# Kernel tuning notes

Measured on AMD Instinct MI355X. Metric: run time of the kernel, lower is better.

## Reference

```python
import jax, jax.numpy as jnp
import numpy as np

N = 100000   # nodes
E = 1600000  # edges
F_IN = 32    # num_features
H = 16       # hidden_size (hardcoded as conv2 input in source)
C = 10       # num_classes
K = 2        # kernel_size (dim=1)


def setup_inputs() -> dict:
    key = jax.random.key(0)
    ks = jax.random.split(key, 9)
    x = jax.random.normal(ks[0], (N, F_IN), dtype=jnp.float32)
    edge_index = jax.random.randint(ks[1], (2, E), 0, N, dtype=jnp.int64)
    edge_attr = jax.random.uniform(ks[2], (E, 1), dtype=jnp.float32)
    s1 = 1.0 / np.sqrt(F_IN)
    s2 = 1.0 / np.sqrt(H)
    W1 = jax.random.normal(ks[3], (K, F_IN, H), dtype=jnp.float32) * s1
    root1 = jax.random.normal(ks[4], (F_IN, H), dtype=jnp.float32) * s1
    b1 = jnp.zeros((H,), dtype=jnp.float32)
    W2 = jax.random.normal(ks[5], (K, H, C), dtype=jnp.float32) * s2
    root2 = jax.random.normal(ks[6], (H, C), dtype=jnp.float32) * s2
    b2 = jnp.zeros((C,), dtype=jnp.float32)
    return {"x": x, "edge_index": edge_index, "edge_attr": edge_attr,
            "W1": W1, "root1": root1, "b1": b1,
            "W2": W2, "root2": root2, "b2": b2}


def spline_conv(x, edge_index, edge_attr, W, root, bias, num_nodes):
    # Open B-spline, degree 1: hat-function basis over K knots.
    k = W.shape[0]
    src, dst = edge_index[0], edge_index[1]
    v = edge_attr[:, 0] * (k - 1)                                   # [E]
    grid = jnp.arange(k, dtype=v.dtype)
    basis = jnp.maximum(0.0, 1.0 - jnp.abs(v[:, None] - grid[None, :]))  # [E,K]
    xe = x[src]                                                      # [E,in] gather
    msg = jnp.einsum('ei,kio,ek->eo', xe, W, basis)                  # per-edge message
    agg = jax.ops.segment_sum(msg, dst, num_segments=num_nodes)      # scatter-add
    deg = jax.ops.segment_sum(jnp.ones((msg.shape[0],), x.dtype), dst,
                              num_segments=num_nodes)
    agg = agg / jnp.maximum(deg, 1.0)[:, None]                       # mean aggregation
    return agg + x @ root + bias


def reference(x, edge_index, edge_attr, W1, root1, b1, W2, root2, b2):
    # Inference mode: F.dropout(training=False) is identity.
    h = jax.nn.elu(spline_conv(x, edge_index, edge_attr, W1, root1, b1, N))
    out = spline_conv(h, edge_index, edge_attr, W2, root2, b2, N)
    return jax.nn.log_softmax(out, axis=1)
```

## Files before the change

### kernel.cpp

```cpp
#include <hip/hip_runtime.h>
#include <math.h>

#define N_NODES 100000
#define E_EDGES 1600000
#define F_IN 32
#define HID 16
#define NC 10
#define SRC_BITS 17
#define SRC_MASK ((1u << SRC_BITS) - 1u)
#define VQ_SCALE 32767.0f
#define CBITS 9
#define BUCKET_N 512
#define NCB ((N_NODES + BUCKET_N - 1) / BUCKET_N)
#define BLK_E 4096
#define NBLK ((E_EDGES + BLK_E - 1) / BLK_E)
#define NODE_GRID ((N_NODES + 255) / 256)

__device__ __forceinline__ unsigned int bf16pair(float lo, float hi) {
    unsigned int ulo = __float_as_uint(lo), uhi = __float_as_uint(hi);
    ulo += 0x7fffu + ((ulo >> 16) & 1u);
    uhi += 0x7fffu + ((uhi >> 16) & 1u);
    return (ulo >> 16) | (uhi & 0xffff0000u);
}

__device__ __forceinline__ float lerp_pair(unsigned int pair, float v) {
    float a = __uint_as_float(pair << 16);
    float b = __uint_as_float(pair & 0xffff0000u);
    return fmaf(v, b - a, a);
}

__global__ __launch_bounds__(256) void fused_l1cnt(
    const float* __restrict__ x, const float* __restrict__ W1,
    const float* __restrict__ root1, const float* __restrict__ b1,
    const int* __restrict__ ei,
    unsigned int* __restrict__ y, float* __restrict__ r1,
    int* __restrict__ cnt)
{
    if (blockIdx.x >= NODE_GRID) {
        __shared__ int h[NCB];
        int b = blockIdx.x - NODE_GRID;
        for (int i = threadIdx.x; i < NCB; i += 256) h[i] = 0;
        __syncthreads();
        int e0 = b * BLK_E;
        for (int i = threadIdx.x; i < BLK_E; i += 256) {
            int e = e0 + i;
            if (e < E_EDGES) atomicAdd(&h[ei[E_EDGES + e] >> CBITS], 1);
        }
        __syncthreads();
        for (int s = threadIdx.x; s < NCB; s += 256)
            cnt[s * NBLK + b] = h[s];
        return;
    }
    __shared__ float sW0[F_IN * HID], sW1[F_IN * HID], sR[F_IN * HID], sB[HID];
    for (int i = threadIdx.x; i < F_IN * HID; i += 256) {
        sW0[i] = W1[i];
        sW1[i] = W1[F_IN * HID + i];
        sR[i]  = root1[i];
    }
    if (threadIdx.x < HID) sB[threadIdx.x] = b1[threadIdx.x];
    __syncthreads();

    int n = blockIdx.x * 256 + threadIdx.x;
    if (n >= N_NODES) return;

    float xr[F_IN];
    const float4* xp = (const float4*)(x + (size_t)n * F_IN);
    #pragma unroll
    for (int i = 0; i < F_IN / 4; i++) {
        float4 t = xp[i];
        xr[i*4+0] = t.x; xr[i*4+1] = t.y; xr[i*4+2] = t.z; xr[i*4+3] = t.w;
    }

    float a0[HID], a1[HID], ar[HID];
    #pragma unroll
    for (int o = 0; o < HID; o++) { a0[o] = 0.f; a1[o] = 0.f; ar[o] = sB[o]; }
    for (int i = 0; i < F_IN; i++) {
        float xi = xr[i];
        #pragma unroll
        for (int o = 0; o < HID; o++) {
            a0[o] += xi * sW0[i * HID + o];
            a1[o] += xi * sW1[i * HID + o];
            ar[o] += xi * sR[i * HID + o];
        }
    }
    unsigned int* py = y + (size_t)n * 16;
    float* pr = r1 + (size_t)n * HID;
    #pragma unroll
    for (int o = 0; o < HID; o++) {
        py[o] = bf16pair(a0[o], a1[o]);
        pr[o] = ar[o];
    }
}

__global__ __launch_bounds__(512) void k_cscan(int* __restrict__ cnt,
                                               int* __restrict__ tsum,
                                               int* __restrict__ start)
{
    __shared__ int lds[512];
    int s = blockIdx.x, t = threadIdx.x;
    int v = (t < NBLK) ? cnt[s * NBLK + t] : 0;
    lds[t] = v;
    __syncthreads();
    #pragma unroll
    for (int off = 1; off < 512; off <<= 1) {
        int u = (t >= off) ? lds[t - off] : 0;
        __syncthreads();
        lds[t] += u;
        __syncthreads();
    }
    if (t < NBLK) cnt[s * NBLK + t] = lds[t] - v;
    if (t == 511) tsum[s] = lds[511];
    if (s == 0 && t == 0) start[N_NODES] = E_EDGES;
}

__global__ __launch_bounds__(256) void k_bucket(
    const int* __restrict__ ei, const float* __restrict__ ea,
    const int* __restrict__ pref, const int* __restrict__ tsum,
    int2* __restrict__ ebuf)
{
    __shared__ int sbb[256];
    __shared__ int base[NCB], cur[NCB];
    int t = threadIdx.x;
    int v = (t < NCB) ? tsum[t] : 0;
    sbb[t] = v;
    __syncthreads();
    #pragma unroll
    for (int off = 1; off < 256; off <<= 1) {
        int u = (t >= off) ? sbb[t - off] : 0;
        __syncthreads();
        sbb[t] += u;
        __syncthreads();
    }
    if (t < NCB) {
        base[t] = (sbb[t] - v) + pref[t * NBLK + blockIdx.x];
        cur[t] = 0;
    }
    __syncthreads();
    int e0 = blockIdx.x * BLK_E;
    for (int i = t; i < BLK_E; i += 256) {
        int e = e0 + i;
        if (e >= E_EDGES) continue;
        int dst = ei[E_EDGES + e];
        int s = dst >> CBITS;
        int off = atomicAdd(&cur[s], 1);
        unsigned int vq = (unsigned int)(ea[e] * VQ_SCALE + 0.5f);
        unsigned int packed = (vq << SRC_BITS) | (unsigned int)ei[e];
        ebuf[base[s] + off] = make_int2(dst & (BUCKET_N - 1), (int)packed);
    }
}

__global__ __launch_bounds__(512) void k_bsort(
    const int2* __restrict__ ebuf, const int* __restrict__ tsum,
    unsigned int* __restrict__ es, int* __restrict__ start)
{
    __shared__ int sbb[256];
    __shared__ int hist[BUCKET_N];
    __shared__ int cursor[BUCKET_N];
    __shared__ int wsum[8], woff[8];
    int t = threadIdx.x;
    int b = blockIdx.x;
    int v = 0;
    if (t < 256) { v = (t < NCB) ? tsum[t] : 0; sbb[t] = v; }
    __syncthreads();
    #pragma unroll
    for (int off = 1; off < 256; off <<= 1) {
        int u = 0;
        if (t < 256 && t >= off) u = sbb[t - off];
        __syncthreads();
        if (t < 256) sbb[t] += u;
        __syncthreads();
    }
    int m  = tsum[b];
    int j0 = sbb[b] - m;
    int j1 = j0 + m;
    hist[t] = 0; cursor[t] = 0;
    __syncthreads();
    for (int j = j0 + t; j < j1; j += 512)
        atomicAdd(&hist[ebuf[j].x], 1);
    __syncthreads();
    int c = hist[t];
    int w = t >> 6, l = t & 63;
    int incl = c;
    #pragma unroll
    for (int off = 1; off < 64; off <<= 1) {
        int u = __shfl_up(incl, off, 64);
        if (l >= off) incl += u;
    }
    if (l == 63) wsum[w] = incl;
    __syncthreads();
    if (t == 0) {
        int acc = 0;
        #pragma unroll
        for (int i = 0; i < 8; i++) { woff[i] = acc; acc += wsum[i]; }
    }
    __syncthreads();
    int excl = woff[w] + incl - c;
    hist[t] = excl;
    int node = (b << CBITS) + t;
    if (node < N_NODES) start[node] = j0 + excl;
    __syncthreads();
    for (int j = j0 + t; j < j1; j += 512) {
        int2 p = ebuf[j];
        int off = atomicAdd(&cursor[p.x], 1);
        es[j0 + hist[p.x] + off] = (unsigned int)p.y;
    }
}

__global__ __launch_bounds__(256) void k_agg1(
    const unsigned int* __restrict__ es, const int* __restrict__ start,
    const unsigned int* __restrict__ y, const float* __restrict__ r1,
    const float* __restrict__ W2, const float* __restrict__ root2,
    const float* __restrict__ b2,
    unsigned int* __restrict__ z, float* __restrict__ r2)
{
    __shared__ float sh[16 * 17];
    __shared__ float sW0[HID * NC], sW1[HID * NC], sRt[HID * NC], sB2[NC];
    int t = threadIdx.x;
    if (t < HID * NC) { sW0[t] = W2[t]; sW1[t] = W2[HID * NC + t]; sRt[t] = root2[t]; }
    if (t >= HID * NC && t < HID * NC + NC) sB2[t - HID * NC] = b2[t - HID * NC];

    int idx = blockIdx.x * 256 + t;
    int n = idx >> 4, o = idx & 15, g = t >> 4;
    if (n < N_NODES) {
        int j0 = start[n], j1 = start[n + 1];
        float acc0 = 0.f, acc1 = 0.f, acc2 = 0.f, acc3 = 0.f;
        int j = j0;
        for (; j + 7 < j1; j += 8) {
            unsigned int p0 = es[j],   p1 = es[j+1], p2 = es[j+2], p3 = es[j+3];
            unsigned int p4 = es[j+4], p5 = es[j+5], p6 = es[j+6], p7 = es[j+7];
            unsigned int q0 = y[(size_t)(p0 & SRC_MASK) * 16 + o];
            unsigned int q1 = y[(size_t)(p1 & SRC_MASK) * 16 + o];
            unsigned int q2 = y[(size_t)(p2 & SRC_MASK) * 16 + o];
            unsigned int q3 = y[(size_t)(p3 & SRC_MASK) * 16 + o];
            unsigned int q4 = y[(size_t)(p4 & SRC_MASK) * 16 + o];
            unsigned int q5 = y[(size_t)(p5 & SRC_MASK) * 16 + o];
            unsigned int q6 = y[(size_t)(p6 & SRC_MASK) * 16 + o];
            unsigned int q7 = y[(size_t)(p7 & SRC_MASK) * 16 + o];
            acc0 += lerp_pair(q0, (float)(p0 >> SRC_BITS) * (1.0f / VQ_SCALE));
            acc1 += lerp_pair(q1, (float)(p1 >> SRC_BITS) * (1.0f / VQ_SCALE));
            acc2 += lerp_pair(q2, (float)(p2 >> SRC_BITS) * (1.0f / VQ_SCALE));
            acc3 += lerp_pair(q3, (float)(p3 >> SRC_BITS) * (1.0f / VQ_SCALE));
            acc0 += lerp_pair(q4, (float)(p4 >> SRC_BITS) * (1.0f / VQ_SCALE));
            acc1 += lerp_pair(q5, (float)(p5 >> SRC_BITS) * (1.0f / VQ_SCALE));
            acc2 += lerp_pair(q6, (float)(p6 >> SRC_BITS) * (1.0f / VQ_SCALE));
            acc3 += lerp_pair(q7, (float)(p7 >> SRC_BITS) * (1.0f / VQ_SCALE));
        }
        for (; j + 3 < j1; j += 4) {
            unsigned int p0 = es[j], p1 = es[j+1], p2 = es[j+2], p3 = es[j+3];
            unsigned int q0 = y[(size_t)(p0 & SRC_MASK) * 16 + o];
            unsigned int q1 = y[(size_t)(p1 & SRC_MASK) * 16 + o];
            unsigned int q2 = y[(size_t)(p2 & SRC_MASK) * 16 + o];
            unsigned int q3 = y[(size_t)(p3 & SRC_MASK) * 16 + o];
            acc0 += lerp_pair(q0, (float)(p0 >> SRC_BITS) * (1.0f / VQ_SCALE));
            acc1 += lerp_pair(q1, (float)(p1 >> SRC_BITS) * (1.0f / VQ_SCALE));
            acc2 += lerp_pair(q2, (float)(p2 >> SRC_BITS) * (1.0f / VQ_SCALE));
            acc3 += lerp_pair(q3, (float)(p3 >> SRC_BITS) * (1.0f / VQ_SCALE));
        }
        for (; j < j1; j++) {
            unsigned int p = es[j];
            unsigned int q = y[(size_t)(p & SRC_MASK) * 16 + o];
            acc0 += lerp_pair(q, (float)(p >> SRC_BITS) * (1.0f / VQ_SCALE));
        }
        float acc = (acc0 + acc1) + (acc2 + acc3);
        float inv = 1.0f / fmaxf((float)(j1 - j0), 1.0f);
        float hv = acc * inv + r1[(size_t)n * HID + o];
        sh[g * 17 + o] = hv > 0.0f ? hv : expm1f(hv);
    }
    __syncthreads();

    int n2 = blockIdx.x * 16 + g;
    if (n2 < N_NODES) {
        int cc = o;
        unsigned int* pz = z + (size_t)n2 * 16;
        if (cc < NC) {
            float a0 = 0.f, a1 = 0.f, ar = sB2[cc];
            #pragma unroll
            for (int i = 0; i < HID; i++) {
                float hi = sh[g * 17 + i];
                a0 += hi * sW0[i * NC + cc];
                a1 += hi * sW1[i * NC + cc];
                ar += hi * sRt[i * NC + cc];
            }
            pz[cc] = bf16pair(a0, a1);
            r2[(size_t)n2 * NC + cc] = ar;
        } else {
            pz[cc] = 0u;
        }
    }
}

__global__ __launch_bounds__(256) void k_agg2(
    const unsigned int* __restrict__ es, const int* __restrict__ start,
    const unsigned int* __restrict__ z,
    const float* __restrict__ r2, float* __restrict__ out)
{
    int idx = blockIdx.x * 256 + threadIdx.x;
    int n = idx >> 4, o = idx & 15;
    if (n >= N_NODES) return;
    int j0 = start[n], j1 = start[n + 1];
    float acc0 = 0.f, acc1 = 0.f, acc2 = 0.f, acc3 = 0.f;
    int j = j0;
    for (; j + 7 < j1; j += 8) {
        unsigned int p0 = es[j],   p1 = es[j+1], p2 = es[j+2], p3 = es[j+3];
        unsigned int p4 = es[j+4], p5 = es[j+5], p6 = es[j+6], p7 = es[j+7];
        unsigned int q0 = z[(size_t)(p0 & SRC_MASK) * 16 + o];
        unsigned int q1 = z[(size_t)(p1 & SRC_MASK) * 16 + o];
        unsigned int q2 = z[(size_t)(p2 & SRC_MASK) * 16 + o];
        unsigned int q3 = z[(size_t)(p3 & SRC_MASK) * 16 + o];
        unsigned int q4 = z[(size_t)(p4 & SRC_MASK) * 16 + o];
        unsigned int q5 = z[(size_t)(p5 & SRC_MASK) * 16 + o];
        unsigned int q6 = z[(size_t)(p6 & SRC_MASK) * 16 + o];
        unsigned int q7 = z[(size_t)(p7 & SRC_MASK) * 16 + o];
        acc0 += lerp_pair(q0, (float)(p0 >> SRC_BITS) * (1.0f / VQ_SCALE));
        acc1 += lerp_pair(q1, (float)(p1 >> SRC_BITS) * (1.0f / VQ_SCALE));
        acc2 += lerp_pair(q2, (float)(p2 >> SRC_BITS) * (1.0f / VQ_SCALE));
        acc3 += lerp_pair(q3, (float)(p3 >> SRC_BITS) * (1.0f / VQ_SCALE));
        acc0 += lerp_pair(q4, (float)(p4 >> SRC_BITS) * (1.0f / VQ_SCALE));
        acc1 += lerp_pair(q5, (float)(p5 >> SRC_BITS) * (1.0f / VQ_SCALE));
        acc2 += lerp_pair(q6, (float)(p6 >> SRC_BITS) * (1.0f / VQ_SCALE));
        acc3 += lerp_pair(q7, (float)(p7 >> SRC_BITS) * (1.0f / VQ_SCALE));
    }
    for (; j + 3 < j1; j += 4) {
        unsigned int p0 = es[j], p1 = es[j+1], p2 = es[j+2], p3 = es[j+3];
        unsigned int q0 = z[(size_t)(p0 & SRC_MASK) * 16 + o];
        unsigned int q1 = z[(size_t)(p1 & SRC_MASK) * 16 + o];
        unsigned int q2 = z[(size_t)(p2 & SRC_MASK) * 16 + o];
        unsigned int q3 = z[(size_t)(p3 & SRC_MASK) * 16 + o];
        acc0 += lerp_pair(q0, (float)(p0 >> SRC_BITS) * (1.0f / VQ_SCALE));
        acc1 += lerp_pair(q1, (float)(p1 >> SRC_BITS) * (1.0f / VQ_SCALE));
        acc2 += lerp_pair(q2, (float)(p2 >> SRC_BITS) * (1.0f / VQ_SCALE));
        acc3 += lerp_pair(q3, (float)(p3 >> SRC_BITS) * (1.0f / VQ_SCALE));
    }
    for (; j < j1; j++) {
        unsigned int p = es[j];
        unsigned int q = z[(size_t)(p & SRC_MASK) * 16 + o];
        acc0 += lerp_pair(q, (float)(p >> SRC_BITS) * (1.0f / VQ_SCALE));
    }
    float acc = (acc0 + acc1) + (acc2 + acc3);
    float val = -INFINITY;
    if (o < NC) {
        float inv = 1.0f / fmaxf((float)(j1 - j0), 1.0f);
        val = acc * inv + r2[(size_t)n * NC + o];
    }
    float mx = val;
    #pragma unroll
    for (int off = 8; off > 0; off >>= 1) mx = fmaxf(mx, __shfl_xor(mx, off, 16));
    float ex = (o < NC) ? expf(val - mx) : 0.0f;
    float ssum = ex;
    #pragma unroll
    for (int off = 8; off > 0; off >>= 1) ssum += __shfl_xor(ssum, off, 16);
    if (o < NC) out[(size_t)n * NC + o] = val - mx - logf(ssum);
}

extern "C" void kernel_launch(void* const* d_in, const int* in_sizes, int n_in,
                              void* d_out, int out_size, void* d_ws, size_t ws_size,
                              hipStream_t stream) {
    const float* x     = (const float*)d_in[0];
    const int*   ei    = (const int*)d_in[1];
    const float* ea    = (const float*)d_in[2];
    const float* W1    = (const float*)d_in[3];
    const float* root1 = (const float*)d_in[4];
    const float* b1    = (const float*)d_in[5];
    const float* W2    = (const float*)d_in[6];
    const float* root2 = (const float*)d_in[7];
    const float* b2    = (const float*)d_in[8];
    float* out = (float*)d_out;

    char* wsb = (char*)d_ws;
    int2*         ebuf   = (int2*)wsb;
    unsigned int* es     = (unsigned int*)(wsb + (size_t)E_EDGES * 8);
    unsigned int* y      = es + (size_t)E_EDGES;
    float*        r1     = (float*)(y + (size_t)N_NODES * 16);
    unsigned int* z      = (unsigned int*)(r1 + (size_t)N_NODES * HID);
    float*        r2     = (float*)(z + (size_t)N_NODES * 16);
    int*          start  = (int*)(r2 + (size_t)N_NODES * NC);
    int*          cnt    = start + N_NODES + 1;
    int*          tsum   = cnt + NCB * NBLK;

    int aggGrid  = (N_NODES * 16 + 255) / 256;

    fused_l1cnt<<<NODE_GRID + NBLK, 256, 0, stream>>>(x, W1, root1, b1, ei, y, r1, cnt);
    k_cscan <<<NCB, 512, 0, stream>>>(cnt, tsum, start);
    k_bucket<<<NBLK, 256, 0, stream>>>(ei, ea, cnt, tsum, ebuf);
    k_bsort <<<NCB, 512, 0, stream>>>(ebuf, tsum, es, start);
    k_agg1  <<<aggGrid, 256, 0, stream>>>(es, start, y, r1, W2, root2, b2, z, r2);
    k_agg2  <<<aggGrid, 256, 0, stream>>>(es, start, z, r2, out);
}
```

Before: 191.8 us.

## Vectorize edge loads, double bucket block size, use wave-shuffle scans

Doubles the per-block edge chunk of the bucket/count passes so there are half as many blocks and prefix entries (NBLK drops to fit 256 threads). The count and bucket kernels read dst, src and edge_attr with 128-bit int4/float4 loads, four edges per thread. The LDS Hillis-Steele scans in k_cscan, k_bucket and k_bsort become wave-level __shfl_up scans plus a small cross-wave combine, cutting barrier count. The bigger blocks mean fewer blocks for the bucket pass, which may lower occupancy and raise LDS atomic contention per block.

```diff
diff --git a/kernel.cpp b/kernel.cpp
--- a/kernel.cpp
+++ b/kernel.cpp
@@ -12,7 +12,7 @@
 #define CBITS 9
 #define BUCKET_N 512
 #define NCB ((N_NODES + BUCKET_N - 1) / BUCKET_N)
-#define BLK_E 4096
+#define BLK_E 8192
 #define NBLK ((E_EDGES + BLK_E - 1) / BLK_E)
 #define NODE_GRID ((N_NODES + 255) / 256)
 
@@ -41,10 +41,20 @@
         int b = blockIdx.x - NODE_GRID;
         for (int i = threadIdx.x; i < NCB; i += 256) h[i] = 0;
         __syncthreads();
+        const int* dstp = ei + E_EDGES;
         int e0 = b * BLK_E;
-        for (int i = threadIdx.x; i < BLK_E; i += 256) {
+        for (int i = threadIdx.x * 4; i < BLK_E; i += 1024) {
             int e = e0 + i;
-            if (e < E_EDGES) atomicAdd(&h[ei[E_EDGES + e] >> CBITS], 1);
+            if (e + 3 < E_EDGES) {
+                int4 d4 = *(const int4*)(dstp + e);
+                atomicAdd(&h[d4.x >> CBITS], 1);
+                atomicAdd(&h[d4.y >> CBITS], 1);
+                atomicAdd(&h[d4.z >> CBITS], 1);
+                atomicAdd(&h[d4.w >> CBITS], 1);
+            } else {
+                for (int k = 0; k < 4; k++)
+                    if (e + k < E_EDGES) atomicAdd(&h[dstp[e + k] >> CBITS], 1);
+            }
         }
         __syncthreads();
         for (int s = threadIdx.x; s < NCB; s += 256)
@@ -92,24 +102,31 @@
     }
 }
 
-__global__ __launch_bounds__(512) void k_cscan(int* __restrict__ cnt,
+__global__ __launch_bounds__(256) void k_cscan(int* __restrict__ cnt,
                                                int* __restrict__ tsum,
                                                int* __restrict__ start)
 {
-    __shared__ int lds[512];
+    __shared__ int wsum[4], woff[4];
     int s = blockIdx.x, t = threadIdx.x;
     int v = (t < NBLK) ? cnt[s * NBLK + t] : 0;
-    lds[t] = v;
-    __syncthreads();
-    #pragma unroll
-    for (int off = 1; off < 512; off <<= 1) {
-        int u = (t >= off) ? lds[t - off] : 0;
-        __syncthreads();
-        lds[t] += u;
-        __syncthreads();
-    }
-    if (t < NBLK) cnt[s * NBLK + t] = lds[t] - v;
-    if (t == 511) tsum[s] = lds[511];
+    int w = t >> 6, l = t & 63;
+    int incl = v;
+    #pragma unroll
+    for (int off = 1; off < 64; off <<= 1) {
+        int u = __shfl_up(incl, off, 64);
+        if (l >= off) incl += u;
+    }
+    if (l == 63) wsum[w] = incl;
+    __syncthreads();
+    if (t == 0) {
+        int a = 0;
+        #pragma unroll
+        for (int i = 0; i < 4; i++) { woff[i] = a; a += wsum[i]; }
+    }
+    __syncthreads();
+    int excl = woff[w] + incl - v;
+    if (t < NBLK) cnt[s * NBLK + t] = excl;
+    if (t == 255) tsum[s] = woff[3] + incl;
     if (s == 0 && t == 0) start[N_NODES] = E_EDGES;
 }
 
@@ -118,34 +135,79 @@
     const int* __restrict__ pref, const int* __restrict__ tsum,
     int2* __restrict__ ebuf)
 {
-    __shared__ int sbb[256];
+    __shared__ int wsum[4], woff[4];
     __shared__ int base[NCB], cur[NCB];
     int t = threadIdx.x;
     int v = (t < NCB) ? tsum[t] : 0;
-    sbb[t] = v;
-    __syncthreads();
-    #pragma unroll
-    for (int off = 1; off < 256; off <<= 1) {
-        int u = (t >= off) ? sbb[t - off] : 0;
-        __syncthreads();
-        sbb[t] += u;
-        __syncthreads();
-    }
+    int w = t >> 6, l = t & 63;
+    int incl = v;
+    #pragma unroll
+    for (int off = 1; off < 64; off <<= 1) {
+        int u = __shfl_up(incl, off, 64);
+        if (l >= off) incl += u;
+    }
+    if (l == 63) wsum[w] = incl;
+    __syncthreads();
+    if (t == 0) {
+        int a = 0;
+        #pragma unroll
+        for (int i = 0; i < 4; i++) { woff[i] = a; a += wsum[i]; }
+    }
+    __syncthreads();
     if (t < NCB) {
-        base[t] = (sbb[t] - v) + pref[t * NBLK + blockIdx.x];
+        base[t] = (woff[w] + incl - v) + pref[t * NBLK + blockIdx.x];
         cur[t] = 0;
     }
     __syncthreads();
+
+    const int* dstp = ei + E_EDGES;
     int e0 = blockIdx.x * BLK_E;
-    for (int i = t; i < BLK_E; i += 256) {
+    for (int i = t * 4; i < BLK_E; i += 1024) {
         int e = e0 + i;
-        if (e >= E_EDGES) continue;
-        int dst = ei[E_EDGES + e];
-        int s = dst >> CBITS;
-        int off = atomicAdd(&cur[s], 1);
-        unsigned int vq = (unsigned int)(ea[e] * VQ_SCALE + 0.5f);
-        unsigned int packed = (vq << SRC_BITS) | (unsigned int)ei[e];
-        ebuf[base[s] + off] = make_int2(dst & (BUCKET_N - 1), (int)packed);
+        if (e + 3 < E_EDGES) {
+            int4 d4 = *(const int4*)(dstp + e);
+            int4 s4 = *(const int4*)(ei + e);
+            float4 a4 = *(const float4*)(ea + e);
+            {
+                int s = d4.x >> CBITS;
+                int off = atomicAdd(&cur[s], 1);
+                unsigned int vq = (unsigned int)(a4.x * VQ_SCALE + 0.5f);
+                ebuf[base[s] + off] = make_int2(d4.x & (BUCKET_N - 1),
+                                               (int)((vq << SRC_BITS) | (unsigned int)s4.x));
+            }
+            {
+                int s = d4.y >> CBITS;
+                int off = atomicAdd(&cur[s], 1);
+                unsigned int vq = (unsigned int)(a4.y * VQ_SCALE + 0.5f);
+                ebuf[base[s] + off] = make_int2(d4.y & (BUCKET_N - 1),
+                                               (int)((vq << SRC_BITS) | (unsigned int)s4.y));
+            }
+            {
+                int s = d4.z >> CBITS;
+                int off = atomicAdd(&cur[s], 1);
+                unsigned int vq = (unsigned int)(a4.z * VQ_SCALE + 0.5f);
+                ebuf[base[s] + off] = make_int2(d4.z & (BUCKET_N - 1),
+                                               (int)((vq << SRC_BITS) | (unsigned int)s4.z));
+            }
+            {
+                int s = d4.w >> CBITS;
+                int off = atomicAdd(&cur[s], 1);
+                unsigned int vq = (unsigned int)(a4.w * VQ_SCALE + 0.5f);
+                ebuf[base[s] + off] = make_int2(d4.w & (BUCKET_N - 1),
+                                               (int)((vq << SRC_BITS) | (unsigned int)s4.w));
+            }
+        } else {
+            for (int k = 0; k < 4; k++) {
+                int ee = e + k;
+                if (ee >= E_EDGES) break;
+                int dst = dstp[ee];
+                int s = dst >> CBITS;
+                int off = atomicAdd(&cur[s], 1);
+                unsigned int vq = (unsigned int)(ea[ee] * VQ_SCALE + 0.5f);
+                ebuf[base[s] + off] = make_int2(dst & (BUCKET_N - 1),
+                                               (int)((vq << SRC_BITS) | (unsigned int)ei[ee]));
+            }
+        }
     }
 }
 
@@ -153,28 +215,35 @@
     const int2* __restrict__ ebuf, const int* __restrict__ tsum,
     unsigned int* __restrict__ es, int* __restrict__ start)
 {
-    __shared__ int sbb[256];
     __shared__ int hist[BUCKET_N];
     __shared__ int cursor[BUCKET_N];
     __shared__ int wsum[8], woff[8];
+    __shared__ int sj0;
     int t = threadIdx.x;
     int b = blockIdx.x;
-    int v = 0;
-    if (t < 256) { v = (t < NCB) ? tsum[t] : 0; sbb[t] = v; }
-    __syncthreads();
-    #pragma unroll
-    for (int off = 1; off < 256; off <<= 1) {
-        int u = 0;
-        if (t < 256 && t >= off) u = sbb[t - off];
+    {
+        int v = (t < NCB) ? tsum[t] : 0;
+        int w = t >> 6, l = t & 63;
+        int incl = v;
+        #pragma unroll
+        for (int off = 1; off < 64; off <<= 1) {
+            int u = __shfl_up(incl, off, 64);
+            if (l >= off) incl += u;
+        }
+        if (l == 63) wsum[w] = incl;
+        hist[t] = 0; cursor[t] = 0;
         __syncthreads();
-        if (t < 256) sbb[t] += u;
+        if (t == 0) {
+            int a = 0;
+            #pragma unroll
+            for (int i = 0; i < 8; i++) { woff[i] = a; a += wsum[i]; }
+        }
         __syncthreads();
+        if (t == b) sj0 = woff[w] + incl - v;
+        __syncthreads();
     }
     int m  = tsum[b];
-    int j0 = sbb[b] - m;
-    int j1 = j0 + m;
-    hist[t] = 0; cursor[t] = 0;
-    __syncthreads();
+    int j0 = sj0, j1 = j0 + m;
     for (int j = j0 + t; j < j1; j += 512)
         atomicAdd(&hist[ebuf[j].x], 1);
     __syncthreads();
@@ -380,7 +449,7 @@
     int aggGrid  = (N_NODES * 16 + 255) / 256;
 
     fused_l1cnt<<<NODE_GRID + NBLK, 256, 0, stream>>>(x, W1, root1, b1, ei, y, r1, cnt);
-    k_cscan <<<NCB, 512, 0, stream>>>(cnt, tsum, start);
+    k_cscan <<<NCB, 256, 0, stream>>>(cnt, tsum, start);
     k_bucket<<<NBLK, 256, 0, stream>>>(ei, ea, cnt, tsum, ebuf);
     k_bsort <<<NCB, 512, 0, stream>>>(ebuf, tsum, es, start);
     k_agg1  <<<aggGrid, 256, 0, stream>>>(es, start, y, r1, W2, root2, b2, z, r2);
```

After: 188.1 us. No clear change (-1.9%).
